# Performance work log

Measured on AMD Instinct MI355X. Metric: run time of the kernel, lower is better.

The kernel has to match this reference:

```python
import jax, jax.numpy as jnp
import numpy as np

D = 1024
B, S = 4, 2048


def setup_inputs() -> dict:
    key = jax.random.key(0)
    ks = jax.random.split(key, 9)
    std = 1.0 / np.sqrt(D)
    x = jax.random.normal(ks[0], (B, S, D), dtype=jnp.float32)
    Wq = jax.random.normal(ks[1], (D, D), dtype=jnp.float32) * std
    bq = jax.random.normal(ks[2], (D,), dtype=jnp.float32) * std
    Wk = jax.random.normal(ks[3], (D, D), dtype=jnp.float32) * std
    bk = jax.random.normal(ks[4], (D,), dtype=jnp.float32) * std
    Wv = jax.random.normal(ks[5], (D, D), dtype=jnp.float32) * std
    bv = jax.random.normal(ks[6], (D,), dtype=jnp.float32) * std
    Wo = jax.random.normal(ks[7], (D, D), dtype=jnp.float32) * std
    bo = jax.random.normal(ks[8], (D,), dtype=jnp.float32) * std
    return {"x": x, "Wq": Wq, "bq": bq, "Wk": Wk, "bk": bk,
            "Wv": Wv, "bv": bv, "Wo": Wo, "bo": bo}


def reference(x, Wq, bq, Wk, bk, Wv, bv, Wo, bo):
    d = x.shape[-1]
    q = x @ Wq + bq          # [B, S, D]
    k = x @ Wk + bk          # [B, S, D] (first call: kv cache empty)
    v = x @ Wv + bv          # [B, S, D]
    scale = 1.0 / jnp.sqrt(jnp.asarray(d, dtype=x.dtype))
    att = jnp.einsum('bqd,bkd->bqk', q, k) * scale  # [B, S, S]
    sq, sk = q.shape[1], k.shape[1]
    causal = jnp.triu(jnp.ones((sq, sk), dtype=bool), k=1)
    att = jnp.where(causal, -jnp.inf, att)
    att = jax.nn.softmax(att, axis=-1)
    out = jnp.einsum('bqk,bkd->bqd', att, v)        # [B, S, D]
    return out @ Wo + bo
```

## Files before the change

### kernel.cpp

```cpp
#include <hip/hip_runtime.h>
#include <hip/hip_bf16.h>


typedef __attribute__((ext_vector_type(8))) __bf16 bf16x8;
typedef __attribute__((ext_vector_type(4))) float f32x4;
typedef __attribute__((ext_vector_type(8))) unsigned short u16x8;
typedef __attribute__((ext_vector_type(4))) float float4v;
typedef long long ll;

static __device__ __forceinline__ unsigned short f2b(float f) {
  unsigned int u = __float_as_uint(f);
  u += 0x7fffu + ((u >> 16) & 1u);
  return (unsigned short)(u >> 16);
}
static __device__ __forceinline__ float b2f(unsigned short b) {
  return __uint_as_float(((unsigned int)b) << 16);
}

static __device__ __forceinline__ void gload16(const unsigned short* g, unsigned short* l) {
  __builtin_amdgcn_global_load_lds(
      (const __attribute__((address_space(1))) void*)g,
      (__attribute__((address_space(3))) void*)l, 16, 0, 0);
}

__global__ __launch_bounds__(256) void cvt_f32_bf16(const float* __restrict__ in,
                                                    unsigned short* __restrict__ out,
                                                    long long n) {
  long long i = ((long long)blockIdx.x * 256 + threadIdx.x) * 8;
  if (i + 8 > n) return;
  float4v a = *(const float4v*)(in + i);
  float4v b = *(const float4v*)(in + i + 4);
  u16x8 o;
  o[0] = f2b(a[0]); o[1] = f2b(a[1]); o[2] = f2b(a[2]); o[3] = f2b(a[3]);
  o[4] = f2b(b[0]); o[5] = f2b(b[1]); o[6] = f2b(b[2]); o[7] = f2b(b[3]);
  *(u16x8*)(out + i) = o;
}

__global__ __launch_bounds__(256) void transpose_cvt(const float* __restrict__ in,
                                                     unsigned short* __restrict__ out, int n) {
  __shared__ float t[32][33];
  int bx = blockIdx.x * 32, by = blockIdx.y * 32;
  int tx = threadIdx.x, ty = threadIdx.y;
#pragma unroll
  for (int i = 0; i < 32; i += 8)
    t[ty + i][tx] = in[(ll)(by + ty + i) * n + bx + tx];
  __syncthreads();
#pragma unroll
  for (int i = 0; i < 32; i += 8)
    out[(ll)(bx + ty + i) * n + by + tx] = f2b(t[tx][ty + i]);
}

__global__ void concat2(const float* __restrict__ a, const float* __restrict__ b,
                        float* __restrict__ o, int n) {
  int i = blockIdx.x * 256 + threadIdx.x;
  if (i < n) { o[i] = a[i]; o[i + n] = b[i]; }
}

template <int CAUSAL>
__global__ __launch_bounds__(256) void gemm_tn(
    const unsigned short* __restrict__ A, const unsigned short* __restrict__ B,
    const float* __restrict__ bias, void* __restrict__ C,
    int K, int lda, int ldb, int ldc,
    ll strideA, ll strideB, ll strideC,
    float alpha, int c_is_bf16, int bias_row) {
  if (CAUSAL == 1 && blockIdx.x > blockIdx.y) return;

  __shared__ unsigned short sA[128][64];
  __shared__ unsigned short sB[128][64];

  const int tid = threadIdx.x;
  const int w = tid >> 6, lane = tid & 63;
  const int bz = blockIdx.z;
  const unsigned short* Ab = A + (ll)bz * strideA;
  const unsigned short* Bb = B + (ll)bz * strideB;
  const int brow = blockIdx.y * 128, bcol = blockIdx.x * 128;
  const int wr = (w >> 1) * 64, wc = (w & 1) * 64;
  const int lr = lane & 15, lk = lane >> 4;

  const int Keff = (CAUSAL == 2) ? (brow + 128) : K;

  f32x4 acc[4][4];
#pragma unroll
  for (int i = 0; i < 4; ++i)
#pragma unroll
    for (int n = 0; n < 4; ++n) acc[i][n] = (f32x4){0.f, 0.f, 0.f, 0.f};

  for (int kb = 0; kb < Keff; kb += 64) {
    __syncthreads();
#pragma unroll
    for (int it = 0; it < 4; ++it) {
      const int chunk = it * 4 + w;
      const int slot = chunk * 64 + lane;
      const int row = slot >> 3, kg = slot & 7;
      gload16(Ab + (ll)(brow + row) * lda + kb + kg * 8, &sA[0][0] + chunk * 512);
      gload16(Bb + (ll)(bcol + row) * ldb + kb + kg * 8, &sB[0][0] + chunk * 512);
    }
    __syncthreads();
#pragma unroll
    for (int kk = 0; kk < 64; kk += 32) {
      const int k0 = kk + lk * 8;
      bf16x8 af[4], bfr[4];
#pragma unroll
      for (int i = 0; i < 4; ++i) af[i] = *(const bf16x8*)&sA[wr + i * 16 + lr][k0];
#pragma unroll
      for (int n = 0; n < 4; ++n) bfr[n] = *(const bf16x8*)&sB[wc + n * 16 + lr][k0];
#pragma unroll
      for (int i = 0; i < 4; ++i)
#pragma unroll
        for (int n = 0; n < 4; ++n)
          acc[i][n] = __builtin_amdgcn_mfma_f32_16x16x32_bf16(af[i], bfr[n], acc[i][n], 0, 0, 0);
    }
  }

  ll cbase = (ll)bz * strideC;
#pragma unroll
  for (int i = 0; i < 4; ++i) {
    int row = brow + wr + i * 16 + lk * 4;
#pragma unroll
    for (int n = 0; n < 4; ++n) {
      int col = bcol + wc + n * 16 + lr;
#pragma unroll
      for (int r = 0; r < 4; ++r) {
        float bvv = bias ? (bias_row ? bias[row + r] : bias[col]) : 0.0f;
        float v = (acc[i][n][r] + bvv) * alpha;
        ll idx = cbase + (ll)(row + r) * ldc + col;
        if (c_is_bf16) ((unsigned short*)C)[idx] = f2b(v);
        else ((float*)C)[idx] = v;
      }
    }
  }
}

__global__ __launch_bounds__(256) void softmax_row2048(unsigned short* __restrict__ S) {
  const int r = blockIdx.x, b = blockIdx.y;
  unsigned short* row = S + ((ll)b * 2048 + r) * 2048;
  const int tid = threadIdx.x;
  const int i0 = tid * 8;
  __shared__ float red[4];

  u16x8 v = *(const u16x8*)(row + i0);
  float f[8];
  float m = -3.0e38f;
#pragma unroll
  for (int j = 0; j < 8; ++j) {
    f[j] = (i0 + j <= r) ? b2f(v[j]) : -3.0e38f;
    m = fmaxf(m, f[j]);
  }
#pragma unroll
  for (int o = 1; o < 64; o <<= 1) m = fmaxf(m, __shfl_xor(m, o, 64));
  if ((tid & 63) == 0) red[tid >> 6] = m;
  __syncthreads();
  m = fmaxf(fmaxf(red[0], red[1]), fmaxf(red[2], red[3]));
  __syncthreads();

  float e[8];
  float s = 0.0f;
#pragma unroll
  for (int j = 0; j < 8; ++j) {
    e[j] = (i0 + j <= r) ? __expf(f[j] - m) : 0.0f;
    s += e[j];
  }
#pragma unroll
  for (int o = 1; o < 64; o <<= 1) s += __shfl_xor(s, o, 64);
  if ((tid & 63) == 0) red[tid >> 6] = s;
  __syncthreads();
  s = red[0] + red[1] + red[2] + red[3];
  float inv = 1.0f / s;
  u16x8 o8;
#pragma unroll
  for (int j = 0; j < 8; ++j) o8[j] = f2b(e[j] * inv);
  *(u16x8*)(row + i0) = o8;
}

extern "C" void kernel_launch(void* const* d_in, const int* in_sizes, int n_in,
                              void* d_out, int out_size, void* d_ws, size_t ws_size,
                              hipStream_t stream) {
  const float* x  = (const float*)d_in[0];
  const float* Wq = (const float*)d_in[1];
  const float* bq = (const float*)d_in[2];
  const float* Wk = (const float*)d_in[3];
  const float* bk = (const float*)d_in[4];
  const float* Wv = (const float*)d_in[5];
  const float* bv = (const float*)d_in[6];
  const float* Wo = (const float*)d_in[7];
  const float* bo = (const float*)d_in[8];

  const int B = 4, S = 2048, D = 1024;
  const ll MS = (ll)B * S;

  char* p = (char*)d_ws;
  unsigned short* xb   = (unsigned short*)p; p += MS * D * 2;
  unsigned short* Wqkt = (unsigned short*)p; p += (ll)2 * D * D * 2;
  unsigned short* Wvt  = (unsigned short*)p; p += (ll)D * D * 2;
  unsigned short* Wot  = (unsigned short*)p; p += (ll)D * D * 2;
  float*          bqkc = (float*)p;          p += 2 * D * 4;
  unsigned short* QKc  = (unsigned short*)p; p += MS * 2 * D * 2;
  unsigned short* Vt   = (unsigned short*)p; p += (ll)D * MS * 2;
  unsigned short* Sm   = (unsigned short*)p; p += (ll)B * S * S * 2;
  unsigned short* At   = (unsigned short*)p; p += MS * D * 2;

  dim3 blk(256);
  dim3 tblk(32, 8);

  cvt_f32_bf16<<<dim3(4096), blk, 0, stream>>>(x, xb, MS * D);
  transpose_cvt<<<dim3(32, 32), tblk, 0, stream>>>(Wq, Wqkt, D);
  transpose_cvt<<<dim3(32, 32), tblk, 0, stream>>>(Wk, Wqkt + (ll)D * D, D);
  transpose_cvt<<<dim3(32, 32), tblk, 0, stream>>>(Wv, Wvt, D);
  transpose_cvt<<<dim3(32, 32), tblk, 0, stream>>>(Wo, Wot, D);
  concat2<<<dim3(4), blk, 0, stream>>>(bq, bk, bqkc, D);

  gemm_tn<0><<<dim3(16, 64, 1), blk, 0, stream>>>(
      xb, Wqkt, bqkc, QKc, D, D, D, 2 * D, 0, 0, 0, 1.0f, 1, 0);

  gemm_tn<0><<<dim3(64, 8, 1), blk, 0, stream>>>(
      Wvt, xb, bv, Vt, D, D, D, (int)MS, 0, 0, 0, 1.0f, 1, 1);

  gemm_tn<1><<<dim3(16, 16, 4), blk, 0, stream>>>(
      QKc, QKc + D, nullptr, Sm, D, 2 * D, 2 * D, S,
      (ll)S * 2 * D, (ll)S * 2 * D, (ll)S * S, 0.03125f, 1, 0);

  softmax_row2048<<<dim3(S, B), blk, 0, stream>>>(Sm);

  gemm_tn<2><<<dim3(8, 16, 4), blk, 0, stream>>>(
      Sm, Vt, nullptr, At, S, S, (int)MS, D,
      (ll)S * S, (ll)S, (ll)S * D, 1.0f, 1, 0);

  gemm_tn<0><<<dim3(8, 64, 1), blk, 0, stream>>>(
      At, Wot, bo, d_out, D, D, D, D, 0, 0, 0, 1.0f, 0, 0);
}
```

Measured before the change: 388.6 us.

## Double-buffer GEMM LDS tiles with XOR swizzle and occupancy hint

Makes the bf16 MFMA GEMM double-buffered: the next K-tile is loaded into a second LDS buffer while the current tile is computed, so each iteration needs one barrier instead of two. The column groups inside each LDS row are XOR-swizzled by row to cut bank conflicts on the fragment reads. It also adds a launch-bounds minimum of 2 blocks per CU. In exchange, LDS use doubles to 64 KB per block, which can limit how many blocks fit on a CU.

```diff
diff --git a/kernel.cpp b/kernel.cpp
--- a/kernel.cpp
+++ b/kernel.cpp
@@ -57,7 +57,7 @@
 }
 
 template <int CAUSAL>
-__global__ __launch_bounds__(256) void gemm_tn(
+__global__ __launch_bounds__(256, 2) void gemm_tn(
     const unsigned short* __restrict__ A, const unsigned short* __restrict__ B,
     const float* __restrict__ bias, void* __restrict__ C,
     int K, int lda, int ldb, int ldc,
@@ -65,8 +65,8 @@
     float alpha, int c_is_bf16, int bias_row) {
   if (CAUSAL == 1 && blockIdx.x > blockIdx.y) return;
 
-  __shared__ unsigned short sA[128][64];
-  __shared__ unsigned short sB[128][64];
+  __shared__ unsigned short sA[2][128][64];
+  __shared__ unsigned short sB[2][128][64];
 
   const int tid = threadIdx.x;
   const int w = tid >> 6, lane = tid & 63;
@@ -78,6 +78,7 @@
   const int lr = lane & 15, lk = lane >> 4;
 
   const int Keff = (CAUSAL == 2) ? (brow + 128) : K;
+  const int nt = Keff >> 6;
 
   f32x4 acc[4][4];
 #pragma unroll
@@ -85,32 +86,46 @@
 #pragma unroll
     for (int n = 0; n < 4; ++n) acc[i][n] = (f32x4){0.f, 0.f, 0.f, 0.f};
 
-  for (int kb = 0; kb < Keff; kb += 64) {
-    __syncthreads();
+  auto STAGE = [&](int buf, int kb) {
 #pragma unroll
     for (int it = 0; it < 4; ++it) {
       const int chunk = it * 4 + w;
       const int slot = chunk * 64 + lane;
-      const int row = slot >> 3, kg = slot & 7;
-      gload16(Ab + (ll)(brow + row) * lda + kb + kg * 8, &sA[0][0] + chunk * 512);
-      gload16(Bb + (ll)(bcol + row) * ldb + kb + kg * 8, &sB[0][0] + chunk * 512);
+      const int row = slot >> 3;
+      const int kg = (slot & 7) ^ (row & 7);
+      gload16(Ab + (ll)(brow + row) * lda + kb + kg * 8, &sA[buf][0][0] + chunk * 512);
+      gload16(Bb + (ll)(bcol + row) * ldb + kb + kg * 8, &sB[buf][0][0] + chunk * 512);
     }
-    __syncthreads();
+  };
+
+  auto COMPUTE = [&](int buf) {
 #pragma unroll
     for (int kk = 0; kk < 64; kk += 32) {
-      const int k0 = kk + lk * 8;
       bf16x8 af[4], bfr[4];
-#pragma unroll
-      for (int i = 0; i < 4; ++i) af[i] = *(const bf16x8*)&sA[wr + i * 16 + lr][k0];
-#pragma unroll
-      for (int n = 0; n < 4; ++n) bfr[n] = *(const bf16x8*)&sB[wc + n * 16 + lr][k0];
+      const int kgb = (kk >> 3) + lk;
+      const int sw = (kgb ^ (lr & 7)) * 8;
+#pragma unroll
+      for (int i = 0; i < 4; ++i) af[i] = *(const bf16x8*)&sA[buf][wr + i * 16 + lr][sw];
+#pragma unroll
+      for (int n = 0; n < 4; ++n) bfr[n] = *(const bf16x8*)&sB[buf][wc + n * 16 + lr][sw];
 #pragma unroll
       for (int i = 0; i < 4; ++i)
 #pragma unroll
         for (int n = 0; n < 4; ++n)
           acc[i][n] = __builtin_amdgcn_mfma_f32_16x16x32_bf16(af[i], bfr[n], acc[i][n], 0, 0, 0);
     }
-  }
+  };
+
+  STAGE(0, 0);
+  __syncthreads();
+  int cur = 0;
+  for (int t = 0; t < nt - 1; ++t) {
+    STAGE(cur ^ 1, (t + 1) << 6);
+    COMPUTE(cur);
+    __syncthreads();
+    cur ^= 1;
+  }
+  COMPUTE(cur);
 
   ll cbase = (ll)bz * strideC;
 #pragma unroll
```

Result: faster. 360.3 us (-7.3%).

## Rewrite GEMM with 256x256 tiles, 4-stage LDS pipeline and swizzled shared memory

Applied to the files above, without the earlier changes.

The shared GEMM kernel moves to 512-thread blocks computing 256x256 output tiles with K-step 32. It adds a 4-deep ring of LDS buffers filled by async global-to-LDS loads, paced by explicit vmcnt waits, and an XOR swizzle on LDS slots to avoid bank conflicts. MFMA sections are wrapped in s_setprio. The aim is to hide global load latency and raise data reuse per tile. In exchange, each block uses 128KB of LDS and many accumulator registers, and the grids become much smaller: the causal QK^T launch has only 36 active blocks per batch.

```diff
diff --git a/kernel.cpp b/kernel.cpp
--- a/kernel.cpp
+++ b/kernel.cpp
@@ -57,7 +57,7 @@
 }
 
 template <int CAUSAL>
-__global__ __launch_bounds__(256) void gemm_tn(
+__global__ __launch_bounds__(512, 2) void gemm_tn(
     const unsigned short* __restrict__ A, const unsigned short* __restrict__ B,
     const float* __restrict__ bias, void* __restrict__ C,
     int K, int lda, int ldb, int ldc,
@@ -65,65 +65,89 @@
     float alpha, int c_is_bf16, int bias_row) {
   if (CAUSAL == 1 && blockIdx.x > blockIdx.y) return;
 
-  __shared__ unsigned short sA[128][64];
-  __shared__ unsigned short sB[128][64];
+  __shared__ unsigned short smem[4 * 16384];
 
   const int tid = threadIdx.x;
-  const int w = tid >> 6, lane = tid & 63;
+  const int wid = tid >> 6, lane = tid & 63;
+  const int wm = wid >> 2, wn = wid & 3;
+  const int lr = lane & 15, lk = lane >> 4;
   const int bz = blockIdx.z;
   const unsigned short* Ab = A + (ll)bz * strideA;
   const unsigned short* Bb = B + (ll)bz * strideB;
-  const int brow = blockIdx.y * 128, bcol = blockIdx.x * 128;
-  const int wr = (w >> 1) * 64, wc = (w & 1) * 64;
-  const int lr = lane & 15, lk = lane >> 4;
-
-  const int Keff = (CAUSAL == 2) ? (brow + 128) : K;
-
-  f32x4 acc[4][4];
-#pragma unroll
-  for (int i = 0; i < 4; ++i)
-#pragma unroll
-    for (int n = 0; n < 4; ++n) acc[i][n] = (f32x4){0.f, 0.f, 0.f, 0.f};
-
-  for (int kb = 0; kb < Keff; kb += 64) {
-    __syncthreads();
-#pragma unroll
-    for (int it = 0; it < 4; ++it) {
-      const int chunk = it * 4 + w;
-      const int slot = chunk * 64 + lane;
-      const int row = slot >> 3, kg = slot & 7;
-      gload16(Ab + (ll)(brow + row) * lda + kb + kg * 8, &sA[0][0] + chunk * 512);
-      gload16(Bb + (ll)(bcol + row) * ldb + kb + kg * 8, &sB[0][0] + chunk * 512);
-    }
-    __syncthreads();
-#pragma unroll
-    for (int kk = 0; kk < 64; kk += 32) {
-      const int k0 = kk + lk * 8;
-      bf16x8 af[4], bfr[4];
-#pragma unroll
-      for (int i = 0; i < 4; ++i) af[i] = *(const bf16x8*)&sA[wr + i * 16 + lr][k0];
-#pragma unroll
-      for (int n = 0; n < 4; ++n) bfr[n] = *(const bf16x8*)&sB[wc + n * 16 + lr][k0];
-#pragma unroll
-      for (int i = 0; i < 4; ++i)
-#pragma unroll
-        for (int n = 0; n < 4; ++n)
-          acc[i][n] = __builtin_amdgcn_mfma_f32_16x16x32_bf16(af[i], bfr[n], acc[i][n], 0, 0, 0);
-    }
-  }
+  const int brow = blockIdx.y * 256, bcol = blockIdx.x * 256;
+
+  const int Keff = (CAUSAL == 2) ? (brow + 256) : K;
+  const int nt = Keff >> 5;
+
+  f32x4 acc[8][4];
+#pragma unroll
+  for (int m = 0; m < 8; ++m)
+#pragma unroll
+    for (int n = 0; n < 4; ++n) acc[m][n] = (f32x4){0.f, 0.f, 0.f, 0.f};
+
+  auto STAGE = [&](int t) {
+    unsigned short* lds = &smem[0] + (t & 3) * 16384;
+    const int kb = t << 5;
+#pragma unroll
+    for (int h = 0; h < 2; ++h) {
+      const int c = wid * 2 + h;
+      const int row = c * 16 + (lane >> 2);
+      const int kg = (lane & 3) ^ (row & 3);
+      gload16(Ab + (ll)(brow + row) * lda + kb + kg * 8, lds + c * 512);
+      gload16(Bb + (ll)(bcol + row) * ldb + kb + kg * 8, lds + 8192 + c * 512);
+    }
+  };
+
+  auto COMPUTE = [&](int t) {
+    const unsigned short* lds = &smem[0] + (t & 3) * 16384;
+    bf16x8 a[8], b[4];
+#pragma unroll
+    for (int n = 0; n < 4; ++n) {
+      const int row = wn * 64 + n * 16 + lr;
+      const int slot = lk ^ (row & 3);
+      b[n] = *(const bf16x8*)(lds + 8192 + row * 32 + slot * 8);
+    }
+#pragma unroll
+    for (int m = 0; m < 8; ++m) {
+      const int row = wm * 128 + m * 16 + lr;
+      const int slot = lk ^ (row & 3);
+      a[m] = *(const bf16x8*)(lds + row * 32 + slot * 8);
+    }
+    __builtin_amdgcn_s_setprio(1);
+#pragma unroll
+    for (int m = 0; m < 8; ++m)
+#pragma unroll
+      for (int n = 0; n < 4; ++n)
+        acc[m][n] = __builtin_amdgcn_mfma_f32_16x16x32_bf16(a[m], b[n], acc[m][n], 0, 0, 0);
+    __builtin_amdgcn_s_setprio(0);
+  };
+
+  STAGE(0); STAGE(1); STAGE(2);
+  for (int t = 0; t < nt - 2; ++t) {
+    asm volatile("s_waitcnt vmcnt(8)" ::: "memory");
+    __builtin_amdgcn_s_barrier();
+    if (t + 3 < nt) STAGE(t + 3);
+    COMPUTE(t);
+  }
+  asm volatile("s_waitcnt vmcnt(4)" ::: "memory");
+  __builtin_amdgcn_s_barrier();
+  COMPUTE(nt - 2);
+  asm volatile("s_waitcnt vmcnt(0)" ::: "memory");
+  __builtin_amdgcn_s_barrier();
+  COMPUTE(nt - 1);
 
   ll cbase = (ll)bz * strideC;
 #pragma unroll
-  for (int i = 0; i < 4; ++i) {
-    int row = brow + wr + i * 16 + lk * 4;
+  for (int m = 0; m < 8; ++m) {
+    const int row0 = brow + wm * 128 + m * 16 + lk * 4;
 #pragma unroll
     for (int n = 0; n < 4; ++n) {
-      int col = bcol + wc + n * 16 + lr;
+      const int col = bcol + wn * 64 + n * 16 + lr;
 #pragma unroll
       for (int r = 0; r < 4; ++r) {
-        float bvv = bias ? (bias_row ? bias[row + r] : bias[col]) : 0.0f;
-        float v = (acc[i][n][r] + bvv) * alpha;
-        ll idx = cbase + (ll)(row + r) * ldc + col;
+        float bvv = bias ? (bias_row ? bias[row0 + r] : bias[col]) : 0.0f;
+        float v = (acc[m][n][r] + bvv) * alpha;
+        ll idx = cbase + (ll)(row0 + r) * ldc + col;
         if (c_is_bf16) ((unsigned short*)C)[idx] = f2b(v);
         else ((float*)C)[idx] = v;
       }
@@ -200,6 +224,7 @@
   unsigned short* At   = (unsigned short*)p; p += MS * D * 2;
 
   dim3 blk(256);
+  dim3 blk512(512);
   dim3 tblk(32, 8);
 
   cvt_f32_bf16<<<dim3(4096), blk, 0, stream>>>(x, xb, MS * D);
@@ -209,22 +234,22 @@
   transpose_cvt<<<dim3(32, 32), tblk, 0, stream>>>(Wo, Wot, D);
   concat2<<<dim3(4), blk, 0, stream>>>(bq, bk, bqkc, D);
 
-  gemm_tn<0><<<dim3(16, 64, 1), blk, 0, stream>>>(
+  gemm_tn<0><<<dim3(8, 32, 1), blk512, 0, stream>>>(
       xb, Wqkt, bqkc, QKc, D, D, D, 2 * D, 0, 0, 0, 1.0f, 1, 0);
 
-  gemm_tn<0><<<dim3(64, 8, 1), blk, 0, stream>>>(
+  gemm_tn<0><<<dim3(32, 4, 1), blk512, 0, stream>>>(
       Wvt, xb, bv, Vt, D, D, D, (int)MS, 0, 0, 0, 1.0f, 1, 1);
 
-  gemm_tn<1><<<dim3(16, 16, 4), blk, 0, stream>>>(
+  gemm_tn<1><<<dim3(8, 8, 4), blk512, 0, stream>>>(
       QKc, QKc + D, nullptr, Sm, D, 2 * D, 2 * D, S,
       (ll)S * 2 * D, (ll)S * 2 * D, (ll)S * S, 0.03125f, 1, 0);
 
   softmax_row2048<<<dim3(S, B), blk, 0, stream>>>(Sm);
 
-  gemm_tn<2><<<dim3(8, 16, 4), blk, 0, stream>>>(
+  gemm_tn<2><<<dim3(4, 8, 4), blk512, 0, stream>>>(
       Sm, Vt, nullptr, At, S, S, (int)MS, D,
       (ll)S * S, (ll)S, (ll)S * D, 1.0f, 1, 0);
 
-  gemm_tn<0><<<dim3(8, 64, 1), blk, 0, stream>>>(
+  gemm_tn<0><<<dim3(4, 32, 1), blk512, 0, stream>>>(
       At, Wot, bo, d_out, D, D, D, D, 0, 0, 0, 1.0f, 0, 0);
 }
```

After: 407.3 us. +4.8%, slower.
